# Kernel tuning notes

Measured on AMD Instinct MI355X. Metric: run time of the kernel, lower is better.

The kernel has to match this reference:

```python
import jax, jax.numpy as jnp
import numpy as np

B, T, N, E = 4, 32, 370, 11840
H, HEADS, DH, L, K = 64, 4, 16, 3, 5

def gelu(x):
    return jax.nn.gelu(x, approximate=False)  # torch default GELU is exact erf

def setup_inputs() -> dict:
    key = jax.random.key(0)
    ks = jax.random.split(key, 18)
    s = 0.05  # keep activations well-scaled
    return {
        "x": jax.random.normal(ks[0], (B, T, N, H), jnp.float32),
        "edge_index": jax.random.randint(ks[1], (2, E), 0, N, dtype=jnp.int32),
        "edge_weight": jax.random.uniform(ks[2], (E,), jnp.float32),
        "W_gcn": jax.random.normal(ks[3], (L, H, H), jnp.float32) * s,
        "b_gcn": jax.random.normal(ks[4], (L, H), jnp.float32) * s,
        "W_gat": jax.random.normal(ks[5], (L, H, HEADS * DH), jnp.float32) * s,
        "att_src": jax.random.normal(ks[6], (L, HEADS, DH), jnp.float32) * s,
        "att_dst": jax.random.normal(ks[7], (L, HEADS, DH), jnp.float32) * s,
        "b_gat": jax.random.normal(ks[8], (L, HEADS * DH), jnp.float32) * s,
        "W_t": jax.random.normal(ks[9], (L, H, H, K), jnp.float32) * s,  # (O,I,K)
        "b_t": jax.random.normal(ks[10], (L, H), jnp.float32) * s,
        "ln_g": jnp.ones((L, H), jnp.float32),
        "ln_b": jnp.zeros((L, H), jnp.float32),
        "W1": jax.random.normal(ks[11], (N * H, 256), jnp.float32) * s,
        "b1": jax.random.normal(ks[12], (256,), jnp.float32) * s,
        "W2": jax.random.normal(ks[13], (256, 64), jnp.float32) * s,
        "b2": jax.random.normal(ks[14], (64,), jnp.float32) * s,
    }

def reference(x, edge_index, edge_weight, W_gcn, b_gcn, W_gat, att_src, att_dst,
              b_gat, W_t, b_t, ln_g, ln_b, W1, b1, W2, b2):
    Bb, Tt, Nn, Ff = x.shape
    G = Bb * Tt
    nL = W_gcn.shape[0]
    heads, dh = att_src.shape[1], att_src.shape[2]
    Hh = heads * dh
    # shared topology across all G graphs; add self-loops (PyG default, fill=1.0)
    src, dst = edge_index[0], edge_index[1]
    loop = jnp.arange(Nn, dtype=src.dtype)
    src2 = jnp.concatenate([src, loop])
    dst2 = jnp.concatenate([dst, loop])
    ew2 = jnp.concatenate([edge_weight, jnp.ones((Nn,), edge_weight.dtype)])
    # symmetric GCN normalization (same for every graph in the batch)
    deg = jnp.zeros((Nn,), x.dtype).at[dst2].add(ew2)
    dis = jnp.where(deg > 0, jax.lax.rsqrt(deg), jnp.zeros_like(deg))
    gnorm = dis[src2] * ew2 * dis[dst2]                       # (E2,)
    h = x.reshape(G, Nn, Ff)
    for l in range(nL):
        # ---- GCNConv: transform -> gather -> weighted scatter-add ----
        hw = h @ W_gcn[l]                                     # (G,N,H)
        msg = hw[:, src2] * gnorm[None, :, None]              # (G,E2,H)
        g = jnp.zeros_like(hw).at[:, dst2].add(msg) + b_gcn[l]
        g = gelu(g)
        # ---- GATConv: per-edge softmax attention over incoming edges ----
        gh = (g @ W_gat[l]).reshape(G, Nn, heads, dh)
        asrc = (gh * att_src[l]).sum(-1)                      # (G,N,heads)
        adst = (gh * att_dst[l]).sum(-1)
        e = jax.nn.leaky_relu(asrc[:, src2] + adst[:, dst2], negative_slope=0.2)
        m = jnp.full((G, Nn, heads), -jnp.inf, e.dtype).at[:, dst2].max(e)
        ex = jnp.exp(e - m[:, dst2])
        den = jnp.zeros((G, Nn, heads), e.dtype).at[:, dst2].add(ex)
        alpha = ex / den[:, dst2]                             # (G,E2,heads)
        msgs = gh[:, src2] * alpha[..., None]                 # (G,E2,heads,dh)
        out = jnp.zeros_like(gh).at[:, dst2].add(msgs).reshape(G, Nn, Hh) + b_gat[l]
        # ---- residual + LayerNorm ----
        r = out + h[..., :Hh]
        mu = r.mean(-1, keepdims=True)
        var = ((r - mu) ** 2).mean(-1, keepdims=True)
        h = (r - mu) * jax.lax.rsqrt(var + 1e-5) * ln_g[l] + ln_b[l]
    # ---- temporal convs over T per (batch, node) ----
    Hc = h.shape[-1]
    xt = h.reshape(Bb, Tt, Nn, Hc).transpose(0, 2, 3, 1).reshape(Bb * Nn, Hc, Tt)
    for l in range(nL):
        c = jax.lax.conv_general_dilated(
            xt, W_t[l], (1,), "SAME", dimension_numbers=("NCH", "OIH", "NCH"))
        xt = gelu(c + b_t[l][None, :, None]) + xt
    z = xt.reshape(Bb, Nn, Hc, Tt).transpose(0, 3, 1, 2).reshape(Bb, Tt, Nn * Hc)
    return gelu(z @ W1 + b1) @ W2 + b2
```

## Files before the change

kernel.cpp:

```cpp
#include <hip/hip_runtime.h>
#include <hip/hip_bf16.h>

#define B_   4
#define T_   32
#define N_   370
#define NP_  384
#define E_   11840
#define E2_  12210
#define H_   64
#define G_   128
#define GN_  47360
#define BN_  1480
#define NH_  23680
#define ECAP 320
#define KCH_ 128
#define NCH_ 185

typedef __hip_bfloat16 bf;
typedef short short8 __attribute__((ext_vector_type(8)));
typedef float f32x4 __attribute__((ext_vector_type(4)));

__device__ __forceinline__ float gelu_f(float x){
  return 0.5f * x * (1.0f + erff(x * 0.7071067811865475f));
}
__device__ __forceinline__ float lrelu(float v){ return v > 0.f ? v : 0.2f * v; }
__device__ __forceinline__ float b2f(bf x){ return __bfloat162float(x); }
__device__ __forceinline__ void store_bf4(bf* p, float4 v){
  bf tmp[4] = {__float2bfloat16(v.x), __float2bfloat16(v.y),
               __float2bfloat16(v.z), __float2bfloat16(v.w)};
  *(ushort4*)p = *(const ushort4*)tmp;
}
__device__ __forceinline__ unsigned pk_bf2(float a, float b){
  bf lo = __float2bfloat16(a), hi = __float2bfloat16(b);
  return (unsigned)*(unsigned short*)&lo | ((unsigned)*(unsigned short*)&hi << 16);
}
__device__ __forceinline__ void load_bf8(const bf* p, float* v){
  uint4 u = *(const uint4*)p;
  unsigned ua[4] = {u.x, u.y, u.z, u.w};
  #pragma unroll
  for (int i = 0; i < 4; ++i){
    v[2*i]   = __uint_as_float(ua[i] << 16);
    v[2*i+1] = __uint_as_float(ua[i] & 0xffff0000u);
  }
}

__global__ __launch_bounds__(1024) void k_degscan(const int* __restrict__ ei,
    const float* __restrict__ ew, float* __restrict__ degG,
    int* __restrict__ offs, int* __restrict__ cursor){
  __shared__ float degS[512];
  __shared__ int cntS[512];
  int tid = threadIdx.x;
  if (tid < 512){ degS[tid] = 0.f; cntS[tid] = 0; }
  __syncthreads();
  for (int e = tid; e < E2_; e += 1024){
    int dst = (e < E_) ? ei[E_ + e] : (e - E_);
    float w = (e < E_) ? ew[e] : 1.0f;
    atomicAdd(&degS[dst], w);
    atomicAdd(&cntS[dst], 1);
  }
  __syncthreads();
  if (tid < N_) degG[tid] = degS[tid];
  if (tid < 64){
    int lane = tid;
    int run = 0;
    for (int c0 = 0; c0 < N_; c0 += 64){
      int n = c0 + lane;
      int v = (n < N_) ? cntS[n] : 0;
      int s = v;
      #pragma unroll
      for (int m = 1; m < 64; m <<= 1){
        int t = __shfl_up(s, m, 64);
        if (lane >= m) s += t;
      }
      int excl = run + s - v;
      if (n < N_){ offs[n] = excl; cursor[n] = excl; }
      run += __shfl(s, 63, 64);
    }
    if (lane == 0) offs[N_] = run;
  }
}

__global__ void k_gfa(const int* __restrict__ ei, const float* __restrict__ ew,
                      const float* __restrict__ deg, int* __restrict__ cursor,
                      int* __restrict__ csr_soff, float* __restrict__ A32,
                      const float* __restrict__ W_gcn, const float* __restrict__ W_gat,
                      bf* __restrict__ WT, const float* __restrict__ Wt,
                      bf* __restrict__ WB){
  int b = blockIdx.x;
  if (b < 48){
    int e = b * 256 + threadIdx.x;
    if (e >= E2_) return;
    int s = (e < E_) ? ei[e] : (e - E_);
    int d = (e < E_) ? ei[E_ + e] : (e - E_);
    float w = (e < E_) ? ew[e] : 1.0f;
    float ds = deg[s] > 0.f ? rsqrtf(deg[s]) : 0.f;
    float dd = deg[d] > 0.f ? rsqrtf(deg[d]) : 0.f;
    float gn = ds * w * dd;
    int pos = atomicAdd(&cursor[d], 1);
    csr_soff[pos] = s << 13;
    atomicAdd(&A32[d * NP_ + s], gn);
  } else if (b < 144){
    int i = (b - 48) * 256 + threadIdx.x;
    int ci = i & 63;
    int co = (i >> 6) & 63;
    int m  = (i >> 12) & 1;
    int l  = i >> 13;
    const float* W = m ? W_gat : W_gcn;
    WT[i] = __float2bfloat16(W[(size_t)(l * 64 + ci) * 64 + co]);
  } else {
    int i = (b - 144) * 256 + threadIdx.x;
    int j = i & 7;
    int r = i >> 3;
    int lane = r & 63;
    int mi = (r >> 6) & 3;
    int t2 = r >> 8;
    int kk = t2 % 10, l = t2 / 10;
    int ho = mi * 16 + (lane & 15);
    int k  = kk >> 1;
    int ci = (kk & 1) * 32 + (lane >> 4) * 8 + j;
    WB[i] = __float2bfloat16(Wt[((l * 64 + ho) * 64 + ci) * 5 + k]);
  }
}

__global__ void k_acvt(const float* __restrict__ A32, bf* __restrict__ A16){
  int i = blockIdx.x * 256 + threadIdx.x;
  float4 v = *(const float4*)&A32[i * 4];
  store_bf4(&A16[i * 4], v);
}

__global__ __launch_bounds__(512, 6) void k_gcn_dense(const float* __restrict__ hin,
    const bf* __restrict__ hin16, const bf* __restrict__ A16,
    const bf* __restrict__ WT, const float* __restrict__ b_gcn,
    const float* __restrict__ att_s, const float* __restrict__ att_d,
    bf* __restrict__ gh16, float* __restrict__ asrc, float* __restrict__ adst){
  __shared__ bf As[64 * 136];
  __shared__ bf Bs[64 * 136];
  __shared__ bf ts[64 * 72];
  int tid = threadIdx.x;
  int b0 = blockIdx.x;
  int xcd = b0 & 7, jj6 = b0 >> 3;
  int g = xcd * 16 + jj6 / 6;
  int m0 = (jj6 % 6) * 64;
  int lane = tid & 63, w = tid >> 6;
  int rg = w >> 1, nh = w & 1;
  int lr = lane & 15, lg = lane >> 4;
  f32x4 acc[2];
  { f32x4 zv = {0.f,0.f,0.f,0.f}; acc[0] = zv; acc[1] = zv; }
  for (int kc = 0; kc < 3; ++kc){
    int u = tid & 15, r = tid >> 4;
    #pragma unroll
    for (int it = 0; it < 2; ++it){
      int row = it * 32 + r;
      *(uint4*)&As[row * 136 + u * 8] =
          *(const uint4*)&A16[(size_t)(m0 + row) * NP_ + kc * 128 + u * 8];
    }
    if (hin16){
      #pragma unroll
      for (int it = 0; it < 2; ++it){
        int nn = (it * 32 + r) * 2;
        int n = kc * 128 + nn;
        ushort4 va = (n < N_) ? *(const ushort4*)&hin16[((size_t)g * N_ + n) * 64 + u * 4]
                              : make_ushort4(0, 0, 0, 0);
        ushort4 vb = (n + 1 < N_) ? *(const ushort4*)&hin16[((size_t)g * N_ + n + 1) * 64 + u * 4]
                                  : make_ushort4(0, 0, 0, 0);
        unsigned wa[4] = {(unsigned)va.x | ((unsigned)vb.x << 16),
                          (unsigned)va.y | ((unsigned)vb.y << 16),
                          (unsigned)va.z | ((unsigned)vb.z << 16),
                          (unsigned)va.w | ((unsigned)vb.w << 16)};
        #pragma unroll
        for (int q = 0; q < 4; ++q)
          *(unsigned*)&Bs[(u * 4 + q) * 136 + nn] = wa[q];
      }
    } else {
      #pragma unroll
      for (int it = 0; it < 2; ++it){
        int nn = (it * 32 + r) * 2;
        int n = kc * 128 + nn;
        float4 v0 = (n < N_) ? *(const float4*)&hin[((size_t)g * N_ + n) * 64 + u * 4]
                             : make_float4(0.f, 0.f, 0.f, 0.f);
        float4 v1 = (n + 1 < N_) ? *(const float4*)&hin[((size_t)g * N_ + n + 1) * 64 + u * 4]
                                 : make_float4(0.f, 0.f, 0.f, 0.f);
        float a0[4] = {v0.x, v0.y, v0.z, v0.w};
        float a1[4] = {v1.x, v1.y, v1.z, v1.w};
        #pragma unroll
        for (int q = 0; q < 4; ++q)
          *(unsigned*)&Bs[(u * 4 + q) * 136 + nn] = pk_bf2(a0[q], a1[q]);
      }
    }
    __syncthreads();
    #pragma unroll
    for (int ks = 0; ks < 4; ++ks){
      short8 af = *(const short8*)&As[(rg * 16 + lr) * 136 + ks * 32 + lg * 8];
      #pragma unroll
      for (int j = 0; j < 2; ++j){
        int nt = nh * 2 + j;
        short8 bfr = *(const short8*)&Bs[(nt * 16 + lr) * 136 + ks * 32 + lg * 8];
        acc[j] = __builtin_amdgcn_mfma_f32_16x16x32_bf16(af, bfr, acc[j], 0, 0, 0);
      }
    }
    __syncthreads();
  }
  #pragma unroll
  for (int j = 0; j < 2; ++j){
    int nt = nh * 2 + j;
    #pragma unroll
    for (int q = 0; q < 4; ++q)
      ts[(rg * 16 + lg * 4 + q) * 72 + nt * 16 + lr] = __float2bfloat16(acc[j][q]);
  }
  __syncthreads();
  f32x4 acc2[2];
  { f32x4 zv = {0.f,0.f,0.f,0.f}; acc2[0] = zv; acc2[1] = zv; }
  #pragma unroll
  for (int ks = 0; ks < 2; ++ks){
    short8 af = *(const short8*)&ts[(rg * 16 + lr) * 72 + ks * 32 + lg * 8];
    #pragma unroll
    for (int j = 0; j < 2; ++j){
      int nt = nh * 2 + j;
      short8 wf = *(const short8*)&WT[(size_t)(nt * 16 + lr) * 64 + ks * 32 + lg * 8];
      acc2[j] = __builtin_amdgcn_mfma_f32_16x16x32_bf16(af, wf, acc2[j], 0, 0, 0);
    }
  }
  __syncthreads();
  #pragma unroll
  for (int j = 0; j < 2; ++j){
    int nt = nh * 2 + j;
    float bv = b_gcn[nt * 16 + lr];
    #pragma unroll
    for (int q = 0; q < 4; ++q){
      float gv = gelu_f(acc2[j][q] + bv);
      ts[(rg * 16 + lg * 4 + q) * 72 + nt * 16 + lr] = __float2bfloat16(gv);
    }
  }
  __syncthreads();
  f32x4 acc3[2];
  { f32x4 zv = {0.f,0.f,0.f,0.f}; acc3[0] = zv; acc3[1] = zv; }
  #pragma unroll
  for (int ks = 0; ks < 2; ++ks){
    short8 af = *(const short8*)&ts[(rg * 16 + lr) * 72 + ks * 32 + lg * 8];
    #pragma unroll
    for (int j = 0; j < 2; ++j){
      int nt = nh * 2 + j;
      short8 wf = *(const short8*)&WT[4096 + (size_t)(nt * 16 + lr) * 64 + ks * 32 + lg * 8];
      acc3[j] = __builtin_amdgcn_mfma_f32_16x16x32_bf16(af, wf, acc3[j], 0, 0, 0);
    }
  }
  #pragma unroll
  for (int j = 0; j < 2; ++j){
    int nt = nh * 2 + j;
    float sa = att_s[nt * 16 + lr];
    float sd = att_d[nt * 16 + lr];
    float ps[4], pd[4];
    #pragma unroll
    for (int q = 0; q < 4; ++q){
      int n = m0 + rg * 16 + lg * 4 + q;
      if (n < N_)
        gh16[((size_t)n * G_ + g) * 64 + nt * 16 + lr] = __float2bfloat16(acc3[j][q]);
      ps[q] = acc3[j][q] * sa;
      pd[q] = acc3[j][q] * sd;
    }
    #pragma unroll
    for (int q = 0; q < 4; ++q){
      ps[q] += __shfl_xor(ps[q], 1, 64); ps[q] += __shfl_xor(ps[q], 2, 64);
      ps[q] += __shfl_xor(ps[q], 4, 64); ps[q] += __shfl_xor(ps[q], 8, 64);
      pd[q] += __shfl_xor(pd[q], 1, 64); pd[q] += __shfl_xor(pd[q], 2, 64);
      pd[q] += __shfl_xor(pd[q], 4, 64); pd[q] += __shfl_xor(pd[q], 8, 64);
    }
    if (lr == 0){
      #pragma unroll
      for (int q = 0; q < 4; ++q){
        int n = m0 + rg * 16 + lg * 4 + q;
        if (n < N_){
          asrc[((size_t)n * G_ + g) * 4 + nt] = ps[q];
          adst[((size_t)n * G_ + g) * 4 + nt] = pd[q];
        }
      }
    }
  }
}

__global__ __launch_bounds__(256) void k_gat_agg(const bf* __restrict__ gh,
    const float* __restrict__ asrc, const float* __restrict__ adst,
    const int* __restrict__ csr_soff, const int* __restrict__ offs,
    const float* __restrict__ b_gat, const float* __restrict__ ln_g,
    const float* __restrict__ ln_b, const float* __restrict__ hin,
    float* __restrict__ hout, bf* __restrict__ h16out){
  __shared__ int sS[ECAP];
  int b0 = blockIdx.x;
  int gg = (b0 & 7) >> 1;
  int n = (b0 >> 3) * 2 + (b0 & 1);
  int tid = threadIdx.x;
  int o0 = offs[n], o1 = offs[n + 1];
  int deg = o1 - o0;
  int cap = deg < ECAP ? deg : ECAP;
  for (int i = tid; i < cap; i += 256) sS[i] = csr_soff[o0 + i];
  __syncthreads();
  int ql = tid >> 3, c8 = tid & 7;
  int g = gg * 32 + ql;
  int head = c8 >> 1;
  int gh4 = g * 4 + head;
  int toff = gg * 2048 + ql * 64 + c8 * 8;
  float adv = adst[n * 512 + gh4];
  float den = 0.f;
  float a[8];
  #pragma unroll
  for (int j = 0; j < 8; ++j) a[j] = 0.f;
  int p = 0;
  for (; p + 2 <= cap; p += 2){
    int s0 = sS[p], s1 = sS[p+1];
    float w0 = __expf(lrelu(asrc[(s0 >> 4) + gh4] + adv));
    float w1 = __expf(lrelu(asrc[(s1 >> 4) + gh4] + adv));
    den += w0 + w1;
    float v0[8], v1[8];
    load_bf8(gh + s0 + toff, v0);
    load_bf8(gh + s1 + toff, v1);
    #pragma unroll
    for (int j = 0; j < 8; ++j) a[j] += w0 * v0[j] + w1 * v1[j];
  }
  for (; p < cap; ++p){
    int sv = sS[p];
    float w0 = __expf(lrelu(asrc[(sv >> 4) + gh4] + adv));
    den += w0;
    float v[8];
    load_bf8(gh + sv + toff, v);
    #pragma unroll
    for (int j = 0; j < 8; ++j) a[j] += w0 * v[j];
  }
  for (int r = cap; r < deg; ++r){
    int sv = csr_soff[o0 + r];
    float w0 = __expf(lrelu(asrc[(sv >> 4) + gh4] + adv));
    den += w0;
    float v[8];
    load_bf8(gh + sv + toff, v);
    #pragma unroll
    for (int j = 0; j < 8; ++j) a[j] += w0 * v[j];
  }
  float inv = 1.f / den;
  float4 bg0 = *(const float4*)&b_gat[c8 * 8];
  float4 bg1 = *(const float4*)&b_gat[c8 * 8 + 4];
  float bb[8] = {bg0.x, bg0.y, bg0.z, bg0.w, bg1.x, bg1.y, bg1.z, bg1.w};
  size_t hbase = ((size_t)g * N_ + n) * 64 + c8 * 8;
  float4 h0 = *(const float4*)&hin[hbase];
  float4 h1 = *(const float4*)&hin[hbase + 4];
  float hh[8] = {h0.x, h0.y, h0.z, h0.w, h1.x, h1.y, h1.z, h1.w};
  float r8[8];
  float s1 = 0.f;
  #pragma unroll
  for (int j = 0; j < 8; ++j){
    r8[j] = a[j] * inv + bb[j] + hh[j];
    s1 += r8[j];
  }
  s1 += __shfl_xor(s1, 1, 64); s1 += __shfl_xor(s1, 2, 64); s1 += __shfl_xor(s1, 4, 64);
  float mu = s1 * (1.f / 64.f);
  float s2 = 0.f;
  #pragma unroll
  for (int j = 0; j < 8; ++j){
    float d = r8[j] - mu;
    s2 += d * d;
  }
  s2 += __shfl_xor(s2, 1, 64); s2 += __shfl_xor(s2, 2, 64); s2 += __shfl_xor(s2, 4, 64);
  float rstd = rsqrtf(s2 * (1.f / 64.f) + 1e-5f);
  float4 lg0 = *(const float4*)&ln_g[c8 * 8];
  float4 lg1 = *(const float4*)&ln_g[c8 * 8 + 4];
  float4 lb0 = *(const float4*)&ln_b[c8 * 8];
  float4 lb1 = *(const float4*)&ln_b[c8 * 8 + 4];
  float lg[8] = {lg0.x, lg0.y, lg0.z, lg0.w, lg1.x, lg1.y, lg1.z, lg1.w};
  float lb[8] = {lb0.x, lb0.y, lb0.z, lb0.w, lb1.x, lb1.y, lb1.z, lb1.w};
  float4 w0v, w1v;
  w0v.x = (r8[0]-mu)*rstd*lg[0]+lb[0]; w0v.y = (r8[1]-mu)*rstd*lg[1]+lb[1];
  w0v.z = (r8[2]-mu)*rstd*lg[2]+lb[2]; w0v.w = (r8[3]-mu)*rstd*lg[3]+lb[3];
  w1v.x = (r8[4]-mu)*rstd*lg[4]+lb[4]; w1v.y = (r8[5]-mu)*rstd*lg[5]+lb[5];
  w1v.z = (r8[6]-mu)*rstd*lg[6]+lb[6]; w1v.w = (r8[7]-mu)*rstd*lg[7]+lb[7];
  *(float4*)&hout[hbase] = w0v;
  *(float4*)&hout[hbase + 4] = w1v;
  bf hv[8] = {__float2bfloat16(w0v.x), __float2bfloat16(w0v.y),
              __float2bfloat16(w0v.z), __float2bfloat16(w0v.w),
              __float2bfloat16(w1v.x), __float2bfloat16(w1v.y),
              __float2bfloat16(w1v.z), __float2bfloat16(w1v.w)};
  *(uint4*)&h16out[hbase] = *(const uint4*)hv;
}

__global__ __launch_bounds__(256) void k_tfuse(const float* __restrict__ h,
    const bf* __restrict__ WB, const float* __restrict__ bt,
    bf* __restrict__ z16){
  __shared__ float xf[32 * 68];
  __shared__ float4 xTgv[36 * 8];
  char* xTg = (char*)xTgv;
  int tid = threadIdx.x;
  int w = tid >> 6, lane = tid & 63;
  int bn = blockIdx.x;
  int b = bn / N_, n = bn - b * N_;
  int lq = lane >> 4, lr = lane & 15;
  #pragma unroll
  for (int r = 0; r < 2; ++r){
    int t = w * 8 + r * 4 + lq;
    int c4 = lr * 4;
    float4 v = *(const float4*)&h[((size_t)(b * T_ + t) * N_ + n) * 64 + c4];
    *(float4*)&xf[t * 68 + c4] = v;
    int row = t + 2;
    bf bv[4] = {__float2bfloat16(v.x), __float2bfloat16(v.y),
                __float2bfloat16(v.z), __float2bfloat16(v.w)};
    int bo = (c4 * 2) ^ ((row & 7) << 4);
    *(uint2*)&xTg[row * 128 + bo] = *(const uint2*)bv;
  }
  if (w == 0){
    int zr = (lq < 2) ? lq : (lq + 32);
    *(uint2*)&xTg[zr * 128 + lr * 8] = make_uint2(0u, 0u);
  }
  __syncthreads();
  for (int l = 0; l < 3; ++l){
    const short8* Wp = (const short8*)(WB + (size_t)l * 20480);
    f32x4 acc[2];
    {
      f32x4 zv = {0.f, 0.f, 0.f, 0.f};
      acc[0] = zv; acc[1] = zv;
    }
    #pragma unroll 2
    for (int kk = 0; kk < 10; ++kk){
      int k = kk >> 1;
      int bbyte = (kk & 1) * 64 + lq * 16;
      short8 bfr[2];
      #pragma unroll
      for (int nj = 0; nj < 2; ++nj){
        int row = nj * 16 + lr + k;
        bfr[nj] = *(const short8*)&xTg[row * 128 + (bbyte ^ ((row & 7) << 4))];
      }
      short8 afr = Wp[(kk * 4 + w) * 64 + lane];
      #pragma unroll
      for (int nj = 0; nj < 2; ++nj)
        acc[nj] = __builtin_amdgcn_mfma_f32_16x16x32_bf16(
            afr, bfr[nj], acc[nj], 0, 0, 0);
    }
    __syncthreads();
    {
      int ho0 = w * 16 + lq * 4;
      float4 bt4 = *(const float4*)&bt[l * 64 + ho0];
      float btv[4] = {bt4.x, bt4.y, bt4.z, bt4.w};
      #pragma unroll
      for (int nj = 0; nj < 2; ++nj){
        int t = nj * 16 + lr;
        float4 xr = *(const float4*)&xf[t * 68 + ho0];
        float xv[4] = {xr.x, xr.y, xr.z, xr.w};
        float ov[4];
        #pragma unroll
        for (int q = 0; q < 4; ++q)
          ov[q] = gelu_f(acc[nj][q] + btv[q]) + xv[q];
        *(float4*)&xf[t * 68 + ho0] = make_float4(ov[0], ov[1], ov[2], ov[3]);
        int row = t + 2;
        bf bvv[4] = {__float2bfloat16(ov[0]), __float2bfloat16(ov[1]),
                     __float2bfloat16(ov[2]), __float2bfloat16(ov[3])};
        *(uint2*)&xTg[row * 128 + ((ho0 * 2) ^ ((row & 7) << 4))] = *(const uint2*)bvv;
      }
    }
    __syncthreads();
  }
  #pragma unroll
  for (int r = 0; r < 2; ++r){
    int t = w * 8 + r * 4 + lq;
    int c4 = lr * 4;
    float4 v = *(const float4*)&xf[t * 68 + c4];
    store_bf4(&z16[(size_t)(b * T_ + t) * NH_ + n * 64 + c4], v);
  }
}

__global__ __launch_bounds__(256) void k_mlp1(const bf* __restrict__ z16,
    const float* __restrict__ W1, float* __restrict__ pbuf){
  __shared__ bf zs[128 * 136];
  __shared__ bf ws[128 * 136];
  int kc = blockIdx.x;
  int ch = blockIdx.y;
  int tid = threadIdx.x;
  int k0 = kc * KCH_;
  {
    int u = tid & 15, r = tid >> 4;
    #pragma unroll
    for (int it = 0; it < 8; ++it){
      int row = it * 16 + r;
      uint4 v = *(const uint4*)&z16[(size_t)row * NH_ + k0 + u * 8];
      *(uint4*)&zs[row * 136 + u * 8] = v;
    }
    #pragma unroll
    for (int it = 0; it < 4; ++it){
      int kp = it * 16 + r;
      const float* w0p = &W1[(size_t)(k0 + kp * 2) * 256 + ch * 128 + u * 8];
      const float* w1p = w0p + 256;
      float4 wa0 = *(const float4*)w0p, wa1 = *(const float4*)(w0p + 4);
      float4 wb0 = *(const float4*)w1p, wb1 = *(const float4*)(w1p + 4);
      float ca[8] = {wa0.x, wa0.y, wa0.z, wa0.w, wa1.x, wa1.y, wa1.z, wa1.w};
      float cb[8] = {wb0.x, wb0.y, wb0.z, wb0.w, wb1.x, wb1.y, wb1.z, wb1.w};
      #pragma unroll
      for (int q = 0; q < 8; ++q){
        int col = u * 8 + q;
        *(unsigned*)&ws[col * 136 + kp * 2] = pk_bf2(ca[q], cb[q]);
      }
    }
  }
  __syncthreads();
  int lane = tid & 63, w = tid >> 6;
  int lr = lane & 15, lg = lane >> 4;
  int wr = w * 32;
  f32x4 acc[2][8];
  #pragma unroll
  for (int mt = 0; mt < 2; ++mt)
    #pragma unroll
    for (int nt = 0; nt < 8; ++nt){
      f32x4 zv = {0.f, 0.f, 0.f, 0.f};
      acc[mt][nt] = zv;
    }
  #pragma unroll
  for (int ks = 0; ks < 4; ++ks){
    short8 af[2], bfr[8];
    #pragma unroll
    for (int mt = 0; mt < 2; ++mt)
      af[mt] = *(const short8*)&zs[(wr + mt * 16 + lr) * 136 + ks * 32 + lg * 8];
    #pragma unroll
    for (int nt = 0; nt < 8; ++nt)
      bfr[nt] = *(const short8*)&ws[(nt * 16 + lr) * 136 + ks * 32 + lg * 8];
    #pragma unroll
    for (int mt = 0; mt < 2; ++mt)
      #pragma unroll
      for (int nt = 0; nt < 8; ++nt)
        acc[mt][nt] = __builtin_amdgcn_mfma_f32_16x16x32_bf16(
            af[mt], bfr[nt], acc[mt][nt], 0, 0, 0);
  }
  float* pb = pbuf + (size_t)kc * 32768 + ch * 128;
  #pragma unroll
  for (int mt = 0; mt < 2; ++mt)
    #pragma unroll
    for (int nt = 0; nt < 8; ++nt){
      int row = wr + mt * 16 + lg * 4;
      int col = nt * 16 + lr;
      #pragma unroll
      for (int q = 0; q < 4; ++q)
        pb[(size_t)(row + q) * 256 + col] = acc[mt][nt][q];
    }
}

__global__ __launch_bounds__(256) void k_mlp2(const float* __restrict__ pbuf,
    const float* __restrict__ b1, const float* __restrict__ W2,
    const float* __restrict__ b2, float* __restrict__ outp){
  __shared__ float a[256];
  __shared__ float red[4][64];
  int row = blockIdx.x, tid = threadIdx.x;
  const float* p = pbuf + (size_t)row * 256 + tid;
  float s0 = 0.f, s1 = 0.f, s2 = 0.f, s3 = 0.f, s4 = 0.f;
  for (int kc = 0; kc < NCH_; kc += 5){
    s0 += p[(size_t)(kc+0) * 32768];
    s1 += p[(size_t)(kc+1) * 32768];
    s2 += p[(size_t)(kc+2) * 32768];
    s3 += p[(size_t)(kc+3) * 32768];
    s4 += p[(size_t)(kc+4) * 32768];
  }
  a[tid] = gelu_f(((s0 + s1) + (s2 + s3)) + s4 + b1[tid]);
  __syncthreads();
  int w = tid >> 6, lane = tid & 63;
  float acc = 0.f;
  #pragma unroll
  for (int i = 0; i < 64; ++i)
    acc += a[w * 64 + i] * W2[(w * 64 + i) * 64 + lane];
  red[w][lane] = acc;
  __syncthreads();
  if (tid < 64)
    outp[row * 64 + tid] = red[0][tid] + red[1][tid] + red[2][tid] + red[3][tid]
                           + b2[tid];
}

extern "C" void kernel_launch(void* const* d_in, const int* in_sizes, int n_in,
                              void* d_out, int out_size, void* d_ws, size_t ws_size,
                              hipStream_t stream){
  const float* x     = (const float*)d_in[0];
  const int*   ei    = (const int*)  d_in[1];
  const float* ew    = (const float*)d_in[2];
  const float* W_gcn = (const float*)d_in[3];
  const float* b_gcn = (const float*)d_in[4];
  const float* W_gat = (const float*)d_in[5];
  const float* att_s = (const float*)d_in[6];
  const float* att_d = (const float*)d_in[7];
  const float* b_gat = (const float*)d_in[8];
  const float* W_t   = (const float*)d_in[9];
  const float* b_t   = (const float*)d_in[10];
  const float* ln_g  = (const float*)d_in[11];
  const float* ln_b  = (const float*)d_in[12];
  const float* W1    = (const float*)d_in[13];
  const float* b1    = (const float*)d_in[14];
  const float* W2    = (const float*)d_in[15];
  const float* b2    = (const float*)d_in[16];
  float* outp = (float*)d_out;

  float* F = (float*)d_ws;
  size_t off = 0;
  float* asrc   = F + off; off += 189440;
  float* adst   = F + off; off += 189440;
  float* degG   = F + off; off += 512;
  float* WTf    = F + off; off += 61440;
  float* h      = F + off; off += 3031040;
  float* bufC   = F + off; off += 3031040;
  float* bufD   = F + off; off += 3031040;
  float* bufE   = F + off; off += 1515520;
  float* pbuf   = F + off; off += (size_t)NCH_ * 32768;
  int* I        = (int*)(F + off);
  int* offs     = I;
  int* cursor   = I + 512;
  int* csr_soff = I + 1024;

  bf* WB     = (bf*)WTf;
  bf* WTT    = (bf*)(WTf + 30720);
  float* A32 = bufC;
  bf* A16    = (bf*)(bufC + 147456);
  bf* gh16   = (bf*)bufD;
  bf* z16    = (bf*)bufD;
  bf* h16    = (bf*)bufE;

  hipMemsetAsync(A32, 0, (size_t)NP_ * NP_ * sizeof(float), stream);

  k_degscan<<<1, 1024, 0, stream>>>(ei, ew, degG, offs, cursor);
  k_gfa<<<384, 256, 0, stream>>>(ei, ew, degG, cursor, csr_soff, A32,
                                 W_gcn, W_gat, WTT, W_t, WB);
  k_acvt<<<144, 256, 0, stream>>>(A32, A16);

  for (int l = 0; l < 3; ++l){
    const float* hin = (l == 0) ? x : h;
    const bf* hin16 = (l == 0) ? (const bf*)nullptr : h16;
    k_gcn_dense<<<768, 512, 0, stream>>>(hin, hin16, A16, WTT + (size_t)l * 8192,
                                         b_gcn + l * 64, att_s + l * 64, att_d + l * 64,
                                         gh16, asrc, adst);
    k_gat_agg<<<1480, 256, 0, stream>>>(gh16, asrc, adst, csr_soff, offs,
                                        b_gat + l * 64, ln_g + l * 64, ln_b + l * 64,
                                        hin, h, h16);
  }

  k_tfuse<<<BN_, 256, 0, stream>>>(h, WB, b_t, z16);

  dim3 g1(NCH_, 2);
  k_mlp1<<<g1, 256, 0, stream>>>(z16, W1, pbuf);
  k_mlp2<<<128, 256, 0, stream>>>(pbuf, b1, W2, b2, outp);
}
```

Before: 297.0 us.

## Fuse last-layer GAT aggregation and LayerNorm into the temporal conv kernel

The final GAT aggregation with residual and LayerNorm now runs inside the temporal-conv kernel. Each block handles one (batch, node) pair across all 32 timesteps and writes the normalized rows straight into shared memory for the MFMA convolutions. This removes one kernel launch and the round trip of the last-layer h through global memory. It also moves z16 to a different buffer so it does not alias gh16, which the fused kernel still reads.

```diff
diff --git a/kernel.cpp b/kernel.cpp
--- a/kernel.cpp
+++ b/kernel.cpp
@@ -379,41 +379,127 @@
   *(uint4*)&h16out[hbase] = *(const uint4*)hv;
 }
 
-__global__ __launch_bounds__(256) void k_tfuse(const float* __restrict__ h,
+__global__ __launch_bounds__(256) void k_gat_tfuse(const bf* __restrict__ gh,
+    const float* __restrict__ asrc, const float* __restrict__ adst,
+    const int* __restrict__ csr_soff, const int* __restrict__ offs,
+    const float* __restrict__ b_gat, const float* __restrict__ ln_g,
+    const float* __restrict__ ln_b, const float* __restrict__ hin,
     const bf* __restrict__ WB, const float* __restrict__ bt,
     bf* __restrict__ z16){
+  __shared__ int sS[ECAP];
   __shared__ float xf[32 * 68];
   __shared__ float4 xTgv[36 * 8];
   char* xTg = (char*)xTgv;
+  int b0 = blockIdx.x;
+  int gg = (b0 & 7) >> 1;
+  int n = (b0 >> 3) * 2 + (b0 & 1);
   int tid = threadIdx.x;
+  int o0 = offs[n], o1 = offs[n + 1];
+  int deg = o1 - o0;
+  int cap = deg < ECAP ? deg : ECAP;
+  for (int i = tid; i < cap; i += 256) sS[i] = csr_soff[o0 + i];
+  __syncthreads();
+  int ql = tid >> 3, c8 = tid & 7;
+  int g = gg * 32 + ql;
+  int head = c8 >> 1;
+  int gh4 = g * 4 + head;
+  int toff = gg * 2048 + ql * 64 + c8 * 8;
+  float adv = adst[n * 512 + gh4];
+  float den = 0.f;
+  float a[8];
+  #pragma unroll
+  for (int j = 0; j < 8; ++j) a[j] = 0.f;
+  int p = 0;
+  for (; p + 2 <= cap; p += 2){
+    int s0 = sS[p], s1 = sS[p+1];
+    float w0 = __expf(lrelu(asrc[(s0 >> 4) + gh4] + adv));
+    float w1 = __expf(lrelu(asrc[(s1 >> 4) + gh4] + adv));
+    den += w0 + w1;
+    float v0[8], v1[8];
+    load_bf8(gh + s0 + toff, v0);
+    load_bf8(gh + s1 + toff, v1);
+    #pragma unroll
+    for (int j = 0; j < 8; ++j) a[j] += w0 * v0[j] + w1 * v1[j];
+  }
+  for (; p < cap; ++p){
+    int sv = sS[p];
+    float w0 = __expf(lrelu(asrc[(sv >> 4) + gh4] + adv));
+    den += w0;
+    float v[8];
+    load_bf8(gh + sv + toff, v);
+    #pragma unroll
+    for (int j = 0; j < 8; ++j) a[j] += w0 * v[j];
+  }
+  for (int r = cap; r < deg; ++r){
+    int sv = csr_soff[o0 + r];
+    float w0 = __expf(lrelu(asrc[(sv >> 4) + gh4] + adv));
+    den += w0;
+    float v[8];
+    load_bf8(gh + sv + toff, v);
+    #pragma unroll
+    for (int j = 0; j < 8; ++j) a[j] += w0 * v[j];
+  }
+  float inv = 1.f / den;
+  float4 bg0 = *(const float4*)&b_gat[c8 * 8];
+  float4 bg1 = *(const float4*)&b_gat[c8 * 8 + 4];
+  float bb[8] = {bg0.x, bg0.y, bg0.z, bg0.w, bg1.x, bg1.y, bg1.z, bg1.w};
+  size_t hbase = ((size_t)g * N_ + n) * 64 + c8 * 8;
+  float4 h0 = *(const float4*)&hin[hbase];
+  float4 h1 = *(const float4*)&hin[hbase + 4];
+  float hh[8] = {h0.x, h0.y, h0.z, h0.w, h1.x, h1.y, h1.z, h1.w};
+  float r8[8];
+  float s1 = 0.f;
+  #pragma unroll
+  for (int j = 0; j < 8; ++j){
+    r8[j] = a[j] * inv + bb[j] + hh[j];
+    s1 += r8[j];
+  }
+  s1 += __shfl_xor(s1, 1, 64); s1 += __shfl_xor(s1, 2, 64); s1 += __shfl_xor(s1, 4, 64);
+  float mu = s1 * (1.f / 64.f);
+  float s2 = 0.f;
+  #pragma unroll
+  for (int j = 0; j < 8; ++j){
+    float d = r8[j] - mu;
+    s2 += d * d;
+  }
+  s2 += __shfl_xor(s2, 1, 64); s2 += __shfl_xor(s2, 2, 64); s2 += __shfl_xor(s2, 4, 64);
+  float rstd = rsqrtf(s2 * (1.f / 64.f) + 1e-5f);
+  float4 lg0 = *(const float4*)&ln_g[c8 * 8];
+  float4 lg1 = *(const float4*)&ln_g[c8 * 8 + 4];
+  float4 lb0 = *(const float4*)&ln_b[c8 * 8];
+  float4 lb1 = *(const float4*)&ln_b[c8 * 8 + 4];
+  float lg[8] = {lg0.x, lg0.y, lg0.z, lg0.w, lg1.x, lg1.y, lg1.z, lg1.w};
+  float lb[8] = {lb0.x, lb0.y, lb0.z, lb0.w, lb1.x, lb1.y, lb1.z, lb1.w};
+  float4 w0v, w1v;
+  w0v.x = (r8[0]-mu)*rstd*lg[0]+lb[0]; w0v.y = (r8[1]-mu)*rstd*lg[1]+lb[1];
+  w0v.z = (r8[2]-mu)*rstd*lg[2]+lb[2]; w0v.w = (r8[3]-mu)*rstd*lg[3]+lb[3];
+  w1v.x = (r8[4]-mu)*rstd*lg[4]+lb[4]; w1v.y = (r8[5]-mu)*rstd*lg[5]+lb[5];
+  w1v.z = (r8[6]-mu)*rstd*lg[6]+lb[6]; w1v.w = (r8[7]-mu)*rstd*lg[7]+lb[7];
+  {
+    int t = ql;
+    *(float4*)&xf[t * 68 + c8 * 8] = w0v;
+    *(float4*)&xf[t * 68 + c8 * 8 + 4] = w1v;
+    int row = t + 2;
+    bf hv[8] = {__float2bfloat16(w0v.x), __float2bfloat16(w0v.y),
+                __float2bfloat16(w0v.z), __float2bfloat16(w0v.w),
+                __float2bfloat16(w1v.x), __float2bfloat16(w1v.y),
+                __float2bfloat16(w1v.z), __float2bfloat16(w1v.w)};
+    int sw = (row & 7) << 4;
+    *(uint2*)&xTg[row * 128 + ((c8 * 16) ^ sw)] = *(const uint2*)&hv[0];
+    *(uint2*)&xTg[row * 128 + (((c8 * 8 + 4) * 2) ^ sw)] = *(const uint2*)&hv[4];
+  }
+  if (tid < 64){
+    int lq0 = tid >> 4, lr0 = tid & 15;
+    int zr = (lq0 < 2) ? lq0 : (lq0 + 32);
+    *(uint2*)&xTg[zr * 128 + lr0 * 8] = make_uint2(0u, 0u);
+  }
+  __syncthreads();
   int w = tid >> 6, lane = tid & 63;
-  int bn = blockIdx.x;
-  int b = bn / N_, n = bn - b * N_;
-  int lq = lane >> 4, lr = lane & 15;
-  #pragma unroll
-  for (int r = 0; r < 2; ++r){
-    int t = w * 8 + r * 4 + lq;
-    int c4 = lr * 4;
-    float4 v = *(const float4*)&h[((size_t)(b * T_ + t) * N_ + n) * 64 + c4];
-    *(float4*)&xf[t * 68 + c4] = v;
-    int row = t + 2;
-    bf bv[4] = {__float2bfloat16(v.x), __float2bfloat16(v.y),
-                __float2bfloat16(v.z), __float2bfloat16(v.w)};
-    int bo = (c4 * 2) ^ ((row & 7) << 4);
-    *(uint2*)&xTg[row * 128 + bo] = *(const uint2*)bv;
-  }
-  if (w == 0){
-    int zr = (lq < 2) ? lq : (lq + 32);
-    *(uint2*)&xTg[zr * 128 + lr * 8] = make_uint2(0u, 0u);
-  }
-  __syncthreads();
+  int lq = lane >> 4, lrc = lane & 15;
   for (int l = 0; l < 3; ++l){
     const short8* Wp = (const short8*)(WB + (size_t)l * 20480);
     f32x4 acc[2];
-    {
-      f32x4 zv = {0.f, 0.f, 0.f, 0.f};
-      acc[0] = zv; acc[1] = zv;
-    }
+    { f32x4 zv = {0.f, 0.f, 0.f, 0.f}; acc[0] = zv; acc[1] = zv; }
     #pragma unroll 2
     for (int kk = 0; kk < 10; ++kk){
       int k = kk >> 1;
@@ -421,7 +507,7 @@
       short8 bfr[2];
       #pragma unroll
       for (int nj = 0; nj < 2; ++nj){
-        int row = nj * 16 + lr + k;
+        int row = nj * 16 + lrc + k;
         bfr[nj] = *(const short8*)&xTg[row * 128 + (bbyte ^ ((row & 7) << 4))];
       }
       short8 afr = Wp[(kk * 4 + w) * 64 + lane];
@@ -437,7 +523,7 @@
       float btv[4] = {bt4.x, bt4.y, bt4.z, bt4.w};
       #pragma unroll
       for (int nj = 0; nj < 2; ++nj){
-        int t = nj * 16 + lr;
+        int t = nj * 16 + lrc;
         float4 xr = *(const float4*)&xf[t * 68 + ho0];
         float xv[4] = {xr.x, xr.y, xr.z, xr.w};
         float ov[4];
@@ -456,9 +542,9 @@
   #pragma unroll
   for (int r = 0; r < 2; ++r){
     int t = w * 8 + r * 4 + lq;
-    int c4 = lr * 4;
+    int c4 = lrc * 4;
     float4 v = *(const float4*)&xf[t * 68 + c4];
-    store_bf4(&z16[(size_t)(b * T_ + t) * NH_ + n * 64 + c4], v);
+    store_bf4(&z16[(size_t)(gg * T_ + t) * NH_ + n * 64 + c4], v);
   }
 }
 
@@ -607,7 +693,7 @@
   float* A32 = bufC;
   bf* A16    = (bf*)(bufC + 147456);
   bf* gh16   = (bf*)bufD;
-  bf* z16    = (bf*)bufD;
+  bf* z16    = (bf*)bufE;
   bf* h16    = (bf*)bufE;
 
   hipMemsetAsync(A32, 0, (size_t)NP_ * NP_ * sizeof(float), stream);
@@ -617,7 +703,7 @@
                                  W_gcn, W_gat, WTT, W_t, WB);
   k_acvt<<<144, 256, 0, stream>>>(A32, A16);
 
-  for (int l = 0; l < 3; ++l){
+  for (int l = 0; l < 2; ++l){
     const float* hin = (l == 0) ? x : h;
     const bf* hin16 = (l == 0) ? (const bf*)nullptr : h16;
     k_gcn_dense<<<768, 512, 0, stream>>>(hin, hin16, A16, WTT + (size_t)l * 8192,
@@ -627,8 +713,12 @@
                                         b_gat + l * 64, ln_g + l * 64, ln_b + l * 64,
                                         hin, h, h16);
   }
-
-  k_tfuse<<<BN_, 256, 0, stream>>>(h, WB, b_t, z16);
+  k_gcn_dense<<<768, 512, 0, stream>>>(h, h16, A16, WTT + (size_t)2 * 8192,
+                                       b_gcn + 2 * 64, att_s + 2 * 64, att_d + 2 * 64,
+                                       gh16, asrc, adst);
+  k_gat_tfuse<<<1480, 256, 0, stream>>>(gh16, asrc, adst, csr_soff, offs,
+                                        b_gat + 2 * 64, ln_g + 2 * 64, ln_b + 2 * 64,
+                                        h, WB, b_t, z16);
 
   dim3 g1(NCH_, 2);
   k_mlp1<<<g1, 256, 0, stream>>>(z16, W1, pbuf);
```

Result: faster. 290.3 us (-2.2%).
